# Performance work log

Measured on AMD Instinct MI355X. Metric: run time of the kernel, lower is better.

The kernel has to match this reference:

```python
import math
import jax, jax.numpy as jnp
import numpy as np

B, L, D = 64, 1024, 64

def setup_inputs() -> dict:
    key = jax.random.key(0)
    k1, k2, k3, k4, k5, k6 = jax.random.split(key, 6)
    return {
        "queries": jax.random.normal(k1, (B, L, D), dtype=jnp.float32),
        "keys": jax.random.normal(k2, (B, L, D), dtype=jnp.float32),
        "values": jax.random.normal(k3, (B, L, D), dtype=jnp.float32),
        "pos_k": jax.random.normal(k4, (L, L, D), dtype=jnp.float32),
        "pos_v": jax.random.normal(k5, (L, L, D), dtype=jnp.float32),
        "valid_lens": jax.random.randint(k6, (B,), 0, L, dtype=jnp.int32),
    }

MASK_VALUE = -1e6  # matches torch source's -1000000.0 fill

def reference(queries, keys, values, pos_k, pos_v, valid_lens):
    d = queries.shape[-1]
    scale = 1.0 / math.sqrt(d)
    # content scores: [B, Lq, Lk]
    scores = jnp.einsum("bqd,bkd->bqk", queries, keys)
    # relative-position scores: contract each query position with its RPR key table
    scores_pos = jnp.einsum("bqd,qkd->bqk", queries, pos_k)
    scores = (scores + scores_pos) * scale
    # mask keys beyond valid_lens[b] with -1e6 (as in sequence_mask), then softmax
    kpos = jnp.arange(scores.shape[-1])
    mask = kpos[None, None, :] < valid_lens[:, None, None]  # [B,1,Lk] -> broadcast
    scores = jnp.where(mask, scores, MASK_VALUE)
    attn = jax.nn.softmax(scores, axis=-1)  # [B, Lq, Lk]
    # dropout prob = 0.0 -> identity
    out = jnp.einsum("bqk,bkd->bqd", attn, values)
    out_pos = jnp.einsum("bqk,qkd->bqd", attn, pos_v)
    return out + out_pos
```

## Files before the change

### kernel.cpp

```cpp
#include <hip/hip_runtime.h>
#include <hip/hip_bf16.h>

typedef __attribute__((ext_vector_type(8))) short bf16x8;
typedef __attribute__((ext_vector_type(4))) float f32x4;

#define B_SZ 64
#define L_SZ 1024
#define D_SZ 64
#define SCALE 0.125f

#define KP 36
#define BPITCH 580
#define SA_SZ 9280

__device__ __forceinline__ short f2bf(float f) {
    union { float f; unsigned u; } v; v.f = f;
    unsigned r = (v.u + 0x7fffu + ((v.u >> 16) & 1u)) >> 16;
    return (short)r;
}

__device__ __forceinline__ bf16x8 cvt8(const float* __restrict__ p) {
    f32x4 a = *(const f32x4*)p;
    f32x4 b = *(const f32x4*)(p + 4);
    bf16x8 r;
    r[0] = f2bf(a[0]); r[1] = f2bf(a[1]); r[2] = f2bf(a[2]); r[3] = f2bf(a[3]);
    r[4] = f2bf(b[0]); r[5] = f2bf(b[1]); r[6] = f2bf(b[2]); r[7] = f2bf(b[3]);
    return r;
}

#define MFMA(A, Bf, C) __builtin_amdgcn_mfma_f32_16x16x32_bf16(A, Bf, C, 0, 0, 0)

__global__ __launch_bounds__(512, 2) void rpr_attn(
    const float* __restrict__ Q, const float* __restrict__ Kt,
    const float* __restrict__ V, const float* __restrict__ PK,
    const float* __restrict__ PV, const int* __restrict__ VLEN,
    float* __restrict__ OUT)
{
    __shared__ float SA[2][SA_SZ];
    __shared__ float lbuf[2][256];

    const int tid = threadIdx.x;
    const int wave = tid >> 6, lane = tid & 63;
    const int g = wave >> 2, r = wave & 3;
    const int lane15 = lane & 15, quad = lane >> 4;
    const int b0 = blockIdx.x * 16;
    const int q0 = blockIdx.y * 16;

    float* sa = SA[g];

    bf16x8 qa[4][2], qp[4][2];
    int vl[4];
#pragma unroll
    for (int j = 0; j < 4; ++j) {
        const int bl = r * 4 + j;
        vl[j] = VLEN[b0 + bl];
        const float* pc = Q + ((b0 + bl) * L_SZ + q0 + lane15) * D_SZ + quad * 8;
        qa[j][0] = cvt8(pc); qa[j][1] = cvt8(pc + 32);
        const float* pp = Q + ((b0 + lane15) * L_SZ + q0 + bl) * D_SZ + quad * 8;
        qp[j][0] = cvt8(pp); qp[j][1] = cvt8(pp + 32);
    }

    f32x4 Oc[4][4], Op[4][4];
#pragma unroll
    for (int j = 0; j < 4; ++j)
#pragma unroll
        for (int nt = 0; nt < 4; ++nt) {
            Oc[j][nt] = (f32x4){0.f, 0.f, 0.f, 0.f};
            Op[j][nt] = (f32x4){0.f, 0.f, 0.f, 0.f};
        }
    float l_acc = 0.f;

    const int tg = r * 64 + lane;
    const int lb = tg >> 4, lq = tg & 15;

    for (int it = 0; it < 16; ++it) {
        const int kb = g * 512 + it * 32;

#pragma unroll
        for (int j = 0; j < 4; ++j) {
            const int ql = r * 4 + j;
#pragma unroll
            for (int c = 0; c < 2; ++c) {
                const float* bp = PK + ((q0 + ql) * L_SZ + kb + c * 16 + lane15) * D_SZ + quad * 8;
                f32x4 acc = (f32x4){0.f, 0.f, 0.f, 0.f};
                acc = MFMA(qp[j][0], cvt8(bp), acc);
                acc = MFMA(qp[j][1], cvt8(bp + 32), acc);
#pragma unroll
                for (int i = 0; i < 4; ++i)
                    sa[(quad * 4 + i) * BPITCH + ql * KP + c * 16 + lane15] = acc[i];
            }
        }
        __syncthreads();

#pragma unroll
        for (int j = 0; j < 4; ++j) {
            const int bl = r * 4 + j;
#pragma unroll
            for (int c = 0; c < 2; ++c) {
                const float* bp = Kt + ((b0 + bl) * L_SZ + kb + c * 16 + lane15) * D_SZ + quad * 8;
                f32x4 acc = (f32x4){0.f, 0.f, 0.f, 0.f};
                acc = MFMA(qa[j][0], cvt8(bp), acc);
                acc = MFMA(qa[j][1], cvt8(bp + 32), acc);
                const int kg = kb + c * 16 + lane15;
#pragma unroll
                for (int i = 0; i < 4; ++i) {
                    const int idx = bl * BPITCH + (quad * 4 + i) * KP + c * 16 + lane15;
                    const float s = (acc[i] + sa[idx]) * SCALE;
                    float e;
                    if (vl[j] == 0)       e = 1.0f;
                    else if (kg < vl[j])  e = __expf(s);
                    else                  e = 0.0f;
                    sa[idx] = e;
                }
            }
        }
        __syncthreads();

        {
            const float* row = sa + lb * BPITCH + lq * KP;
            float s = 0.f;
#pragma unroll
            for (int kk = 0; kk < 32; kk += 4) {
                f32x4 v4 = *(const f32x4*)(row + kk);
                s += v4[0] + v4[1] + v4[2] + v4[3];
            }
            l_acc += s;
        }
#pragma unroll
        for (int j = 0; j < 4; ++j) {
            const int bl = r * 4 + j;
            const bf16x8 af = cvt8(sa + bl * BPITCH + lane15 * KP + quad * 8);
            const float* vb = V + ((b0 + bl) * L_SZ + kb + quad * 8) * D_SZ + lane15;
#pragma unroll
            for (int nt = 0; nt < 4; ++nt) {
                bf16x8 bf;
#pragma unroll
                for (int jj = 0; jj < 8; ++jj) bf[jj] = f2bf(vb[jj * D_SZ + nt * 16]);
                Oc[j][nt] = MFMA(af, bf, Oc[j][nt]);
            }
        }
#pragma unroll
        for (int j = 0; j < 4; ++j) {
            const int ql = r * 4 + j;
            const bf16x8 af = cvt8(sa + lane15 * BPITCH + ql * KP + quad * 8);
            const float* vb = PV + ((q0 + ql) * L_SZ + kb + quad * 8) * D_SZ + lane15;
#pragma unroll
            for (int nt = 0; nt < 4; ++nt) {
                bf16x8 bf;
#pragma unroll
                for (int jj = 0; jj < 8; ++jj) bf[jj] = f2bf(vb[jj * D_SZ + nt * 16]);
                Op[j][nt] = MFMA(af, bf, Op[j][nt]);
            }
        }
        __syncthreads();
    }

    lbuf[g][tg] = l_acc;
    float* Obuf = &SA[0][0];

    if (g == 0) {
#pragma unroll
        for (int j = 0; j < 4; ++j)
#pragma unroll
            for (int nt = 0; nt < 4; ++nt)
#pragma unroll
                for (int i = 0; i < 4; ++i)
                    Obuf[((r * 4 + j) * 16 + quad * 4 + i) * 64 + nt * 16 + lane15] = Oc[j][nt][i];
    }
    __syncthreads();
    if (g == 1) {
#pragma unroll
        for (int j = 0; j < 4; ++j)
#pragma unroll
            for (int nt = 0; nt < 4; ++nt)
#pragma unroll
                for (int i = 0; i < 4; ++i)
                    Obuf[((r * 4 + j) * 16 + quad * 4 + i) * 64 + nt * 16 + lane15] += Oc[j][nt][i];
    }
    __syncthreads();
    if (g == 0) {
#pragma unroll
        for (int j = 0; j < 4; ++j)
#pragma unroll
            for (int nt = 0; nt < 4; ++nt)
#pragma unroll
                for (int i = 0; i < 4; ++i)
                    Obuf[((quad * 4 + i) * 16 + r * 4 + j) * 64 + nt * 16 + lane15] += Op[j][nt][i];
    }
    __syncthreads();
    if (g == 1) {
#pragma unroll
        for (int j = 0; j < 4; ++j)
#pragma unroll
            for (int nt = 0; nt < 4; ++nt)
#pragma unroll
                for (int i = 0; i < 4; ++i)
                    Obuf[((quad * 4 + i) * 16 + r * 4 + j) * 64 + nt * 16 + lane15] += Op[j][nt][i];
    }
    __syncthreads();

    for (int idx = tid; idx < 4096; idx += 512) {
        const int d4 = idx & 15, ql2 = (idx >> 4) & 15, bl2 = idx >> 8;
        const float li = lbuf[0][bl2 * 16 + ql2] + lbuf[1][bl2 * 16 + ql2];
        const float rl = 1.0f / li;
        f32x4 o = *(const f32x4*)&Obuf[(bl2 * 16 + ql2) * 64 + d4 * 4];
        o[0] *= rl; o[1] *= rl; o[2] *= rl; o[3] *= rl;
        *(f32x4*)&OUT[((b0 + bl2) * L_SZ + q0 + ql2) * D_SZ + d4 * 4] = o;
    }
}

extern "C" void kernel_launch(void* const* d_in, const int* in_sizes, int n_in,
                              void* d_out, int out_size, void* d_ws, size_t ws_size,
                              hipStream_t stream) {
    (void)in_sizes; (void)n_in; (void)out_size; (void)d_ws; (void)ws_size;
    const float* Q  = (const float*)d_in[0];
    const float* K  = (const float*)d_in[1];
    const float* V  = (const float*)d_in[2];
    const float* PK = (const float*)d_in[3];
    const float* PV = (const float*)d_in[4];
    const int*   VL = (const int*)d_in[5];
    float* OUT = (float*)d_out;

    dim3 grid(4, 64, 1);
    dim3 block(512, 1, 1);
    rpr_attn<<<grid, block, 0, stream>>>(Q, K, V, PK, PV, VL, OUT);
}
```

Before: 1.017 ms.

## Pre-convert inputs to bf16 with transposed V tables and swizzled LDS

Adds pre-pass kernels that convert Q, K and pos_k to bf16 and write V and pos_v transposed in bf16 into the workspace. The main kernel then loads MFMA operands directly as 16-byte vectors instead of gathering and converting fp32 elementwise. It also stores probabilities as bf16 in a separate XOR-swizzled LDS buffer, keeps row sums in registers, and remaps block indices. The cost is an extra full read/write pass over the 256MB position tables per call, plus a fallback path if the workspace is too small.

```diff
diff --git a/kernel.cpp b/kernel.cpp
--- a/kernel.cpp
+++ b/kernel.cpp
@@ -8,10 +8,6 @@
 #define L_SZ 1024
 #define D_SZ 64
 #define SCALE 0.125f
-
-#define KP 36
-#define BPITCH 580
-#define SA_SZ 9280
 
 __device__ __forceinline__ short f2bf(float f) {
     union { float f; unsigned u; } v; v.f = f;
@@ -29,6 +25,239 @@
 }
 
 #define MFMA(A, Bf, C) __builtin_amdgcn_mfma_f32_16x16x32_bf16(A, Bf, C, 0, 0, 0)
+
+__global__ void cvt_bf16_k(const float* __restrict__ src, short* __restrict__ dst, int n8) {
+    const int stride = gridDim.x * blockDim.x;
+    for (int i = blockIdx.x * blockDim.x + threadIdx.x; i < n8; i += stride) {
+        *(bf16x8*)(dst + (size_t)i * 8) = cvt8(src + (size_t)i * 8);
+    }
+}
+
+#define TP 72
+__global__ void tr64_bf16_k(const float* __restrict__ src, short* __restrict__ dst) {
+    __shared__ __attribute__((aligned(16))) short tile[64 * TP];
+    const int kt = blockIdx.x;
+    const size_t o = blockIdx.y;
+    const int tid = threadIdx.x;
+    {
+        const int rr = tid >> 2, c0 = (tid & 3) << 4;
+        const float* sp = src + (o * L_SZ + (size_t)(kt * 64 + rr)) * D_SZ + c0;
+        *(bf16x8*)(tile + rr * TP + c0)     = cvt8(sp);
+        *(bf16x8*)(tile + rr * TP + c0 + 8) = cvt8(sp + 8);
+    }
+    __syncthreads();
+    {
+        const int d = tid >> 2, k4 = (tid & 3) << 4;
+        bf16x8 o0, o1;
+#pragma unroll
+        for (int j = 0; j < 8; ++j) {
+            o0[j] = tile[(k4 + j) * TP + d];
+            o1[j] = tile[(k4 + 8 + j) * TP + d];
+        }
+        short* dp = dst + (o * 64 + (size_t)d) * L_SZ + kt * 64 + k4;
+        *(bf16x8*)dp       = o0;
+        *(bf16x8*)(dp + 8) = o1;
+    }
+}
+
+__global__ __launch_bounds__(512, 2) void rpr_attn_bf16(
+    const short* __restrict__ Qb, const short* __restrict__ Kb,
+    const short* __restrict__ Vt, const short* __restrict__ PKb,
+    const short* __restrict__ PVt, const int* __restrict__ VLEN,
+    float* __restrict__ OUT)
+{
+    __shared__ __attribute__((aligned(16))) float SA[2][256 * 32];
+    __shared__ __attribute__((aligned(16))) short PB[2][256 * 64];
+
+    const int tid = threadIdx.x;
+    const int wave = tid >> 6, lane = tid & 63;
+    const int g = wave >> 2, r = wave & 3;
+    const int lane15 = lane & 15, quad = lane >> 4;
+
+    const int n = blockIdx.x;
+    const int l = (n & 7) * 32 + (n >> 3);
+    const int b0 = (l & 3) * 16;
+    const int q0 = (l >> 2) * 16;
+
+    char* sa = (char*)&SA[g][0];
+    char* pb = (char*)&PB[g][0];
+
+    bf16x8 qa[4][2], qp[4][2];
+    int vl[4];
+#pragma unroll
+    for (int j = 0; j < 4; ++j) {
+        const int bl = r * 4 + j;
+        vl[j] = VLEN[b0 + bl];
+        const short* pc = Qb + ((b0 + bl) * L_SZ + q0 + lane15) * D_SZ + quad * 8;
+        qa[j][0] = *(const bf16x8*)pc;
+        qa[j][1] = *(const bf16x8*)(pc + 32);
+        const short* pp = Qb + ((b0 + lane15) * L_SZ + q0 + bl) * D_SZ + quad * 8;
+        qp[j][0] = *(const bf16x8*)pp;
+        qp[j][1] = *(const bf16x8*)(pp + 32);
+    }
+
+    f32x4 Oc[4][4], Op[4][4];
+    float es[4][4];
+#pragma unroll
+    for (int j = 0; j < 4; ++j)
+#pragma unroll
+        for (int nt = 0; nt < 4; ++nt) {
+            Oc[j][nt] = (f32x4){0.f, 0.f, 0.f, 0.f};
+            Op[j][nt] = (f32x4){0.f, 0.f, 0.f, 0.f};
+            es[j][nt] = 0.f;
+        }
+
+    for (int it = 0; it < 16; ++it) {
+        const int kb = g * 512 + it * 32;
+
+#pragma unroll
+        for (int j = 0; j < 4; ++j) {
+            const int ql = r * 4 + j;
+#pragma unroll
+            for (int c = 0; c < 2; ++c) {
+                const short* bp = PKb + ((q0 + ql) * L_SZ + kb + c * 16 + lane15) * D_SZ + quad * 8;
+                f32x4 acc = (f32x4){0.f, 0.f, 0.f, 0.f};
+                acc = MFMA(qp[j][0], *(const bf16x8*)bp, acc);
+                acc = MFMA(qp[j][1], *(const bf16x8*)(bp + 32), acc);
+#pragma unroll
+                for (int i = 0; i < 4; ++i) {
+                    const int brow = quad * 4 + i;
+                    const int off = (((brow * 16 + ql) * 32 + c * 16 + lane15) * 4)
+                                    ^ (((brow ^ ql) & 7) << 4);
+                    *(float*)(sa + off) = acc[i];
+                }
+            }
+        }
+        __syncthreads();
+
+#pragma unroll
+        for (int j = 0; j < 4; ++j) {
+            const int bl = r * 4 + j;
+#pragma unroll
+            for (int c = 0; c < 2; ++c) {
+                const short* bp = Kb + ((b0 + bl) * L_SZ + kb + c * 16 + lane15) * D_SZ + quad * 8;
+                f32x4 acc = (f32x4){0.f, 0.f, 0.f, 0.f};
+                acc = MFMA(qa[j][0], *(const bf16x8*)bp, acc);
+                acc = MFMA(qa[j][1], *(const bf16x8*)(bp + 32), acc);
+                const int kg = kb + c * 16 + lane15;
+#pragma unroll
+                for (int i = 0; i < 4; ++i) {
+                    const int q = quad * 4 + i;
+                    const int soff = (((bl * 16 + q) * 32 + c * 16 + lane15) * 4)
+                                     ^ (((bl ^ q) & 7) << 4);
+                    const float s = (acc[i] + *(const float*)(sa + soff)) * SCALE;
+                    float e;
+                    if (vl[j] == 0)       e = 1.0f;
+                    else if (kg < vl[j])  e = __expf(s);
+                    else                  e = 0.0f;
+                    es[j][i] += e;
+                    const int poff = (((bl * 16 + q) * 64 + c * 16 + lane15) * 2)
+                                     ^ (((bl ^ q) & 7) << 4);
+                    *(short*)(pb + poff) = f2bf(e);
+                }
+            }
+        }
+        __syncthreads();
+
+#pragma unroll
+        for (int j = 0; j < 4; ++j) {
+            const int bl = r * 4 + j;
+            const int aoff = (((bl * 16 + lane15) * 64) * 2 + quad * 16)
+                             ^ (((bl ^ lane15) & 7) << 4);
+            const bf16x8 af = *(const bf16x8*)(pb + aoff);
+            const short* vb = Vt + ((b0 + bl) * 64 + lane15) * L_SZ + kb + quad * 8;
+#pragma unroll
+            for (int nt = 0; nt < 4; ++nt) {
+                const bf16x8 bf = *(const bf16x8*)(vb + nt * 16 * L_SZ);
+                Oc[j][nt] = MFMA(af, bf, Oc[j][nt]);
+            }
+        }
+#pragma unroll
+        for (int j = 0; j < 4; ++j) {
+            const int ql = r * 4 + j;
+            const int aoff = (((lane15 * 16 + ql) * 64) * 2 + quad * 16)
+                             ^ (((lane15 ^ ql) & 7) << 4);
+            const bf16x8 af = *(const bf16x8*)(pb + aoff);
+            const short* vb = PVt + ((q0 + ql) * 64 + lane15) * L_SZ + kb + quad * 8;
+#pragma unroll
+            for (int nt = 0; nt < 4; ++nt) {
+                const bf16x8 bf = *(const bf16x8*)(vb + nt * 16 * L_SZ);
+                Op[j][nt] = MFMA(af, bf, Op[j][nt]);
+            }
+        }
+        __syncthreads();
+    }
+
+    float* lball = (float*)&PB[0][0];
+#pragma unroll
+    for (int j = 0; j < 4; ++j)
+#pragma unroll
+        for (int i = 0; i < 4; ++i) {
+            float s = es[j][i];
+            s += __shfl_xor(s, 1);
+            s += __shfl_xor(s, 2);
+            s += __shfl_xor(s, 4);
+            s += __shfl_xor(s, 8);
+            if (lane15 == 0)
+                lball[g * 256 + (r * 4 + j) * 16 + quad * 4 + i] = s;
+        }
+
+    float* Obuf = &SA[0][0];
+
+    if (g == 0) {
+#pragma unroll
+        for (int j = 0; j < 4; ++j)
+#pragma unroll
+            for (int nt = 0; nt < 4; ++nt)
+#pragma unroll
+                for (int i = 0; i < 4; ++i)
+                    Obuf[((r * 4 + j) * 16 + quad * 4 + i) * 64 + nt * 16 + lane15] = Oc[j][nt][i];
+    }
+    __syncthreads();
+    if (g == 1) {
+#pragma unroll
+        for (int j = 0; j < 4; ++j)
+#pragma unroll
+            for (int nt = 0; nt < 4; ++nt)
+#pragma unroll
+                for (int i = 0; i < 4; ++i)
+                    Obuf[((r * 4 + j) * 16 + quad * 4 + i) * 64 + nt * 16 + lane15] += Oc[j][nt][i];
+    }
+    __syncthreads();
+    if (g == 0) {
+#pragma unroll
+        for (int j = 0; j < 4; ++j)
+#pragma unroll
+            for (int nt = 0; nt < 4; ++nt)
+#pragma unroll
+                for (int i = 0; i < 4; ++i)
+                    Obuf[((quad * 4 + i) * 16 + r * 4 + j) * 64 + nt * 16 + lane15] += Op[j][nt][i];
+    }
+    __syncthreads();
+    if (g == 1) {
+#pragma unroll
+        for (int j = 0; j < 4; ++j)
+#pragma unroll
+            for (int nt = 0; nt < 4; ++nt)
+#pragma unroll
+                for (int i = 0; i < 4; ++i)
+                    Obuf[((quad * 4 + i) * 16 + r * 4 + j) * 64 + nt * 16 + lane15] += Op[j][nt][i];
+    }
+    __syncthreads();
+
+    for (int idx = tid; idx < 4096; idx += 512) {
+        const int d4 = idx & 15, ql2 = (idx >> 4) & 15, bl2 = idx >> 8;
+        const float li = lball[bl2 * 16 + ql2] + lball[256 + bl2 * 16 + ql2];
+        const float rl = 1.0f / li;
+        f32x4 o = *(const f32x4*)&Obuf[(bl2 * 16 + ql2) * 64 + d4 * 4];
+        o[0] *= rl; o[1] *= rl; o[2] *= rl; o[3] *= rl;
+        *(f32x4*)&OUT[((b0 + bl2) * L_SZ + q0 + ql2) * D_SZ + d4 * 4] = o;
+    }
+}
+
+#define KP 36
+#define BPITCH 580
+#define SA_SZ 9280
 
 __global__ __launch_bounds__(512, 2) void rpr_attn(
     const float* __restrict__ Q, const float* __restrict__ Kt,
@@ -212,7 +441,7 @@
 extern "C" void kernel_launch(void* const* d_in, const int* in_sizes, int n_in,
                               void* d_out, int out_size, void* d_ws, size_t ws_size,
                               hipStream_t stream) {
-    (void)in_sizes; (void)n_in; (void)out_size; (void)d_ws; (void)ws_size;
+    (void)in_sizes; (void)n_in; (void)out_size;
     const float* Q  = (const float*)d_in[0];
     const float* K  = (const float*)d_in[1];
     const float* V  = (const float*)d_in[2];
@@ -221,7 +450,25 @@
     const int*   VL = (const int*)d_in[5];
     float* OUT = (float*)d_out;
 
-    dim3 grid(4, 64, 1);
-    dim3 block(512, 1, 1);
-    rpr_attn<<<grid, block, 0, stream>>>(Q, K, V, PK, PV, VL, OUT);
-}
+    const size_t WS_NEEDED = (3ull * 4194304ull + 2ull * 67108864ull) * 2ull;
+
+    if (d_ws != nullptr && ws_size >= WS_NEEDED) {
+        short* Qb  = (short*)d_ws;
+        short* Kb  = Qb + 4194304;
+        short* Vt  = Kb + 4194304;
+        short* PKb = Vt + 4194304;
+        short* PVt = PKb + 67108864;
+
+        cvt_bf16_k<<<dim3(1024), dim3(256), 0, stream>>>(Q, Qb, 524288);
+        cvt_bf16_k<<<dim3(1024), dim3(256), 0, stream>>>(K, Kb, 524288);
+        cvt_bf16_k<<<dim3(2048), dim3(256), 0, stream>>>(PK, PKb, 8388608);
+        tr64_bf16_k<<<dim3(16, 64),   dim3(256), 0, stream>>>(V, Vt);
+        tr64_bf16_k<<<dim3(16, 1024), dim3(256), 0, stream>>>(PV, PVt);
+
+        rpr_attn_bf16<<<dim3(256), dim3(512), 0, stream>>>(Qb, Kb, Vt, PKb, PVt, VL, OUT);
+    } else {
+        dim3 grid(4, 64, 1);
+        dim3 block(512, 1, 1);
+        rpr_attn<<<grid, block, 0, stream>>>(Q, K, V, PK, PV, VL, OUT);
+    }
+}
```

After: 1.259 ms. 23.8% more time.
